# Kernel optimization log

Hardware: AMD Instinct MI355X
Metric: run time of the kernel (lower is better)

## Reference

```python
import jax, jax.numpy as jnp
import numpy as np

D_MODEL = 512
D_FF = 2048
N_EXPERTS = 8
TOP_K = 2
AUX_COEF = 0.01
Z_COEF = 1e-4
N_LAYERS = 12
INIT_STD = 0.02


def setup_inputs() -> dict:
    key = jax.random.key(0)
    kx, kr, k1, k2, k3 = jax.random.split(key, 5)
    std2 = INIT_STD / np.sqrt(2 * N_LAYERS)  # scale_init_by_depth for w2
    x = jax.random.normal(kx, (4, 1024, D_MODEL), dtype=jnp.float32)
    router_w = jax.random.normal(kr, (D_MODEL, N_EXPERTS), dtype=jnp.float32) * 0.02
    w1 = jax.random.normal(k1, (N_EXPERTS, D_MODEL, D_FF), dtype=jnp.float32) * INIT_STD
    w2 = jax.random.normal(k2, (N_EXPERTS, D_FF, D_MODEL), dtype=jnp.float32) * std2
    w3 = jax.random.normal(k3, (N_EXPERTS, D_MODEL, D_FF), dtype=jnp.float32) * INIT_STD
    return {"x": x, "router_w": router_w, "w1": w1, "w2": w2, "w3": w3}


def reference(x, router_w, w1, w2, w3):
    B, S, D = x.shape
    xf = x.reshape(-1, D)                              # [N, D]
    n_tokens = xf.shape[0]

    router_logits = xf @ router_w                      # [N, E]
    probs = jax.nn.softmax(router_logits.astype(jnp.float32), axis=-1)
    topk_w, topk_i = jax.lax.top_k(probs, TOP_K)       # [N, K]
    topk_w = topk_w / jnp.sum(topk_w, axis=-1, keepdims=True)

    # combine weight per (token, expert): zero for non-selected experts
    combine = jnp.sum(jax.nn.one_hot(topk_i, N_EXPERTS, dtype=jnp.float32)
                      * topk_w[..., None], axis=1)     # [N, E]

    # SwiGLU per expert, masked combine (same math as sorted grouped GEMM + scatter-add)
    gate = jax.nn.silu(jnp.einsum('nd,edf->enf', xf, w1))   # [E, N, F]
    up = jnp.einsum('nd,edf->enf', xf, w3)                  # [E, N, F]
    expert_out = jnp.einsum('enf,efd->end', gate * up, w2)  # [E, N, D]
    out = jnp.einsum('end,ne->nd', expert_out, combine.astype(x.dtype))

    # losses
    importance = probs.mean(axis=0)                    # [E]
    load = jax.nn.one_hot(topk_i[:, 0], N_EXPERTS, dtype=jnp.float32).mean(axis=0)
    aux_loss = N_EXPERTS * jnp.sum(importance * load) * AUX_COEF
    z_loss = jnp.mean(router_logits.astype(jnp.float32) ** 2) * Z_COEF

    return out.reshape(B, S, D), aux_loss, z_loss
```

## Files before the change

### kernel.cpp

```cpp
#include <hip/hip_runtime.h>
#include <hip/hip_fp16.h>

#define D_MODEL 512
#define D_FF    2048
#define NEXP    8
#define NTOK    4096
#define NPAIR   8192
#define DUMMY   NPAIR
#define LSTRIDE 4224
#define MAXTILES 72

typedef _Float16 half8  __attribute__((ext_vector_type(8)));
typedef _Float16 half2v __attribute__((ext_vector_type(2)));
typedef float    f32x4  __attribute__((ext_vector_type(4)));

__device__ __forceinline__ void gload16(const void* g, void* l) {
  __builtin_amdgcn_global_load_lds(
      (const __attribute__((address_space(1))) unsigned*)g,
      (__attribute__((address_space(3))) unsigned*)l, 16, 0, 0);
}

__global__ void k_trans3(const float* __restrict__ w1, const float* __restrict__ w3,
                         const float* __restrict__ w2, _Float16* __restrict__ w1t,
                         _Float16* __restrict__ w3t, _Float16* __restrict__ w2t) {
  __shared__ float t[64][65];
  int bt = blockIdx.x;
  const float* src; _Float16* dst; int R, C, rb, cb;
  if (bt < 4096) {
    src = (bt < 2048) ? w1 : w3; dst = (bt < 2048) ? w1t : w3t;
    int tt = bt & 2047; int e = tt >> 8; int rem = tt & 255;
    R = D_MODEL; C = D_FF; rb = (rem >> 5) * 64; cb = (rem & 31) * 64;
    src += (size_t)e * R * C; dst += (size_t)e * R * C;
  } else {
    int tt = bt - 4096; int e = tt >> 8; int rem = tt & 255;
    src = w2; dst = w2t;
    R = D_FF; C = D_MODEL; rb = (rem >> 3) * 64; cb = (rem & 7) * 64;
    src += (size_t)e * R * C; dst += (size_t)e * R * C;
  }
  int tid = threadIdx.x;
  int tx = tid & 15, ty = tid >> 4;
#pragma unroll
  for (int i = 0; i < 4; i++) {
    float4 v = *(const float4*)(src + (size_t)(rb + ty + i * 16) * C + cb + tx * 4);
    t[ty + i * 16][tx * 4 + 0] = v.x;
    t[ty + i * 16][tx * 4 + 1] = v.y;
    t[ty + i * 16][tx * 4 + 2] = v.z;
    t[ty + i * 16][tx * 4 + 3] = v.w;
  }
  __syncthreads();
  int tx2 = tid & 31, ty2 = tid >> 5;
#pragma unroll
  for (int i = 0; i < 8; i++) {
    int c = ty2 + i * 8;
    int r = tx2 * 2;
    half2v p = {(_Float16)t[r][c], (_Float16)t[r + 1][c]};
    *(half2v*)(dst + (size_t)(cb + c) * R + rb + r) = p;
  }
}

__global__ __launch_bounds__(256) void k_route1(
    const float* __restrict__ x, const float* __restrict__ rw,
    _Float16* __restrict__ xb, int* __restrict__ topE, float* __restrict__ wcomb,
    float* __restrict__ blk, int* __restrict__ ntiles) {
  __shared__ float s_imp[NEXP];
  __shared__ float s_z;
  int tid = threadIdx.x;
  if (tid < NEXP) s_imp[tid] = 0.f;
  if (tid == 0) s_z = 0.f;
  if (blockIdx.x == 0 && tid == 0) ntiles[0] = 0;
  __syncthreads();
  int wave = tid >> 6, lane = tid & 63;
  int n = blockIdx.x * 4 + wave;
  const float* xr = x + (size_t)n * D_MODEL;
  float acc[8] = {0, 0, 0, 0, 0, 0, 0, 0};
  float4 v0 = *(const float4*)(xr + lane * 8);
  float4 v1 = *(const float4*)(xr + lane * 8 + 4);
  float xs[8] = {v0.x, v0.y, v0.z, v0.w, v1.x, v1.y, v1.z, v1.w};
  half8 hx = {(_Float16)xs[0], (_Float16)xs[1], (_Float16)xs[2], (_Float16)xs[3],
              (_Float16)xs[4], (_Float16)xs[5], (_Float16)xs[6], (_Float16)xs[7]};
  *(half8*)(xb + (size_t)n * D_MODEL + lane * 8) = hx;
#pragma unroll
  for (int j = 0; j < 8; j++) {
    const float4* w4 = (const float4*)(rw + (size_t)(lane * 8 + j) * NEXP);
    float4 wa = w4[0], wb = w4[1];
    acc[0] += xs[j] * wa.x; acc[1] += xs[j] * wa.y;
    acc[2] += xs[j] * wa.z; acc[3] += xs[j] * wa.w;
    acc[4] += xs[j] * wb.x; acc[5] += xs[j] * wb.y;
    acc[6] += xs[j] * wb.z; acc[7] += xs[j] * wb.w;
  }
#pragma unroll
  for (int off = 32; off >= 1; off >>= 1) {
#pragma unroll
    for (int e = 0; e < 8; e++) acc[e] += __shfl_xor(acc[e], off);
  }
  if (lane == 0) {
    float z = 0.f;
#pragma unroll
    for (int e = 0; e < 8; e++) z += acc[e] * acc[e];
    float m = acc[0];
#pragma unroll
    for (int e = 1; e < 8; e++) m = fmaxf(m, acc[e]);
    float p[8], s = 0.f;
#pragma unroll
    for (int e = 0; e < 8; e++) { p[e] = expf(acc[e] - m); s += p[e]; }
    float inv = 1.f / s;
#pragma unroll
    for (int e = 0; e < 8; e++) p[e] *= inv;
    int e0 = 0; float p0 = p[0];
#pragma unroll
    for (int e = 1; e < 8; e++) if (p[e] > p0) { p0 = p[e]; e0 = e; }
    int e1 = -1; float p1 = -1.f;
#pragma unroll
    for (int e = 0; e < 8; e++) if (e != e0 && p[e] > p1) { p1 = p[e]; e1 = e; }
    float wsum = p0 + p1;
    topE[n] = e0 | (e1 << 4);
    wcomb[2 * n] = p0 / wsum;
    wcomb[2 * n + 1] = p1 / wsum;
#pragma unroll
    for (int e = 0; e < 8; e++) atomicAdd(&s_imp[e], p[e]);
    atomicAdd(&s_z, z);
  }
  __syncthreads();
  if (tid < 8) blk[blockIdx.x * 9 + tid] = s_imp[tid];
  if (tid == 8) blk[blockIdx.x * 9 + 8] = s_z;
}

__global__ __launch_bounds__(1024) void k_scatter(
    const int* __restrict__ topE, int* __restrict__ lists,
    int* __restrict__ tiletab, int* __restrict__ ntiles,
    int* __restrict__ loadc_g) {
  int e = blockIdx.x;
  __shared__ int wcount[16];
  __shared__ int lcw[16];
  __shared__ int sbase;
  __shared__ int stot;
  int tid = threadIdx.x, lane = tid & 63, wv = tid >> 6;
  if (lane == 0) lcw[wv] = 0;
  int total = 0;
  for (int c = 0; c < 8; c++) {
    int idx = c * 1024 + tid;
    int te = topE[idx >> 1];
    int ee = (idx & 1) ? ((te >> 4) & 15) : (te & 15);
    bool mine = (ee == e);
    unsigned long long bal = __ballot(mine);
    unsigned long long balL = __ballot(mine && !(idx & 1));
    int rank = __popcll(bal & ((1ull << lane) - 1ull));
    if (lane == 0) {
      wcount[wv] = __popcll(bal);
      lcw[wv] += __popcll(balL);
    }
    __syncthreads();
    int pre = total;
    for (int w2 = 0; w2 < wv; w2++) pre += wcount[w2];
    if (mine) lists[e * LSTRIDE + pre + rank] = idx;
    int t16 = 0;
#pragma unroll
    for (int w2 = 0; w2 < 16; w2++) t16 += wcount[w2];
    __syncthreads();
    total += t16;
  }
  int tiles = (total + 127) >> 7;
  if (tid == 0) {
    int lc = 0;
#pragma unroll
    for (int w2 = 0; w2 < 16; w2++) lc += lcw[w2];
    loadc_g[e] = lc;
    sbase = atomicAdd(ntiles, tiles);
    stot = total;
  }
  __syncthreads();
  if (tid < tiles) tiletab[sbase + tid] = e | (tid << 8);
  if (tid < 128) {
    int p = stot + tid;
    if (p < tiles * 128) lists[e * LSTRIDE + p] = DUMMY;
  }
}

__global__ __launch_bounds__(1024) void k_losses(
    const float* __restrict__ blk, const int* __restrict__ loadc_g,
    float* __restrict__ out) {
  __shared__ float fin[9];
  int tid = threadIdx.x, lane = tid & 63, wv = tid >> 6;
  if (wv < 9) {
    float s = 0.f;
    for (int b = lane; b < 1024; b += 64) s += blk[b * 9 + wv];
#pragma unroll
    for (int off = 32; off >= 1; off >>= 1) s += __shfl_xor(s, off);
    if (lane == 0) fin[wv] = s;
  }
  __syncthreads();
  if (tid == 0) {
    float a = 0.f;
#pragma unroll
    for (int e = 0; e < 8; e++)
      a += (fin[e] * (1.f / 4096.f)) * ((float)loadc_g[e] * (1.f / 4096.f));
    out[NTOK * D_MODEL] = 8.f * a * 0.01f;
    out[NTOK * D_MODEL + 1] = fin[8] * (1.f / (4096.f * 8.f)) * 1e-4f;
  }
}

__global__ __launch_bounds__(256) void k_gemm1(
    const _Float16* __restrict__ xb, const _Float16* __restrict__ w1t,
    const _Float16* __restrict__ w3t, _Float16* __restrict__ h,
    const int* __restrict__ lists, const int* __restrict__ tiletab,
    const int* __restrict__ ntiles) {
  int ti = blockIdx.y;
  if (ti >= ntiles[0]) return;
  int ent = tiletab[ti];
  int e = ent & 15, mt = ent >> 8, nt = blockIdx.x;
  __shared__ __align__(16) _Float16 As[2][128 * 32];
  __shared__ __align__(16) _Float16 B1s[2][128 * 32];
  __shared__ __align__(16) _Float16 B3s[2][128 * 32];
  __shared__ int toks[128];
  int tid = threadIdx.x, lane = tid & 63, w = tid >> 6;
  if (tid < 128) toks[tid] = lists[e * LSTRIDE + mt * 128 + tid];
  __syncthreads();
  const _Float16* w1e = w1t + (size_t)e * D_FF * D_MODEL;
  const _Float16* w3e = w3t + (size_t)e * D_FF * D_MODEL;
  int n0 = nt * 128;
  const _Float16 *aS[2], *b1S[2], *b3S[2];
  int ldso[2];
#pragma unroll
  for (int c = 0; c < 2; c++) {
    int rt = w * 32 + c * 16 + (lane >> 2);
    int cg = (lane & 3) ^ ((rt >> 1) & 3);
    aS[c] = xb + (size_t)(toks[rt] >> 1) * D_MODEL + cg * 8;
    b1S[c] = w1e + (size_t)(n0 + rt) * D_MODEL + cg * 8;
    b3S[c] = w3e + (size_t)(n0 + rt) * D_MODEL + cg * 8;
    ldso[c] = (w * 32 + c * 16) * 32;
  }
  f32x4 acc1[4][4] = {};
  f32x4 acc3[4][4] = {};
  int wr = (w >> 1) * 64, wc = (w & 1) * 64;
  int aoff[4], boff[4];
#pragma unroll
  for (int i = 0; i < 4; i++) {
    int r = wr + i * 16 + (lane & 15);
    aoff[i] = r * 32 + (((lane >> 4) ^ ((r >> 1) & 3)) << 3);
    int rb = wc + i * 16 + (lane & 15);
    boff[i] = rb * 32 + (((lane >> 4) ^ ((rb >> 1) & 3)) << 3);
  }
#pragma unroll
  for (int c = 0; c < 2; c++) {
    gload16(aS[c], &As[0][ldso[c]]);
    gload16(b1S[c], &B1s[0][ldso[c]]);
    gload16(b3S[c], &B3s[0][ldso[c]]);
  }
  __syncthreads();
#pragma unroll
  for (int t = 0; t < 16; t++) {
    const int buf = t & 1;
    if (t < 15) {
      const int k1 = (t + 1) * 32;
#pragma unroll
      for (int c = 0; c < 2; c++) {
        gload16(aS[c] + k1, &As[buf ^ 1][ldso[c]]);
        gload16(b1S[c] + k1, &B1s[buf ^ 1][ldso[c]]);
        gload16(b3S[c] + k1, &B3s[buf ^ 1][ldso[c]]);
      }
    }
    half8 af[4], b1f[4], b3f[4];
#pragma unroll
    for (int i = 0; i < 4; i++) {
      af[i] = *(const half8*)(&As[buf][aoff[i]]);
      b1f[i] = *(const half8*)(&B1s[buf][boff[i]]);
      b3f[i] = *(const half8*)(&B3s[buf][boff[i]]);
    }
#pragma unroll
    for (int i = 0; i < 4; i++) {
#pragma unroll
      for (int j = 0; j < 4; j++) {
        acc1[i][j] = __builtin_amdgcn_mfma_f32_16x16x32_f16(af[i], b1f[j], acc1[i][j], 0, 0, 0);
        acc3[i][j] = __builtin_amdgcn_mfma_f32_16x16x32_f16(af[i], b3f[j], acc3[i][j], 0, 0, 0);
      }
    }
    __syncthreads();
  }
#pragma unroll
  for (int i = 0; i < 4; i++) {
    int rbase = wr + i * 16 + ((lane >> 4) << 2);
#pragma unroll
    for (int r = 0; r < 4; r++) {
      int m = rbase + r;
      int pair = toks[m];
      _Float16* hrow = h + (size_t)pair * D_FF + n0 + wc;
#pragma unroll
      for (int j = 0; j < 4; j++) {
        float g = acc1[i][j][r], u = acc3[i][j][r];
        float val = (g / (1.f + __expf(-g))) * u;
        hrow[j * 16 + (lane & 15)] = (_Float16)val;
      }
    }
  }
}

__global__ __launch_bounds__(256) void k_gemm2(
    const _Float16* __restrict__ h, const _Float16* __restrict__ w2t,
    float* __restrict__ pairout, const int* __restrict__ lists,
    const int* __restrict__ tiletab, const int* __restrict__ ntiles,
    const float* __restrict__ wcomb) {
  int ti = blockIdx.y;
  if (ti >= ntiles[0]) return;
  int ent = tiletab[ti];
  int e = ent & 15, mt = ent >> 8, nt = blockIdx.x;
  __shared__ __align__(16) _Float16 As[2][128 * 32];
  __shared__ __align__(16) _Float16 Bs[2][64 * 32];
  __shared__ int toks[128];
  __shared__ float wcs[128];
  int tid = threadIdx.x, lane = tid & 63, w = tid >> 6;
  if (tid < 128) {
    int p = lists[e * LSTRIDE + mt * 128 + tid];
    toks[tid] = p;
    wcs[tid] = (p < NPAIR) ? wcomb[p] : 0.f;
  }
  __syncthreads();
  const _Float16* w2e = w2t + (size_t)e * D_MODEL * D_FF;
  int n0 = nt * 64;
  const _Float16 *aS[2], *bS;
  int ldsa[2], ldsb;
#pragma unroll
  for (int c = 0; c < 2; c++) {
    int rt = w * 32 + c * 16 + (lane >> 2);
    int cg = (lane & 3) ^ ((rt >> 1) & 3);
    aS[c] = h + (size_t)toks[rt] * D_FF + cg * 8;
    ldsa[c] = (w * 32 + c * 16) * 32;
  }
  {
    int rt = w * 16 + (lane >> 2);
    int cg = (lane & 3) ^ ((rt >> 1) & 3);
    bS = w2e + (size_t)(n0 + rt) * D_FF + cg * 8;
    ldsb = (w * 16) * 32;
  }
  f32x4 acc[4][2] = {};
  int wr = (w >> 1) * 64, wc = (w & 1) * 32;
  int aoff[4], boff[2];
#pragma unroll
  for (int i = 0; i < 4; i++) {
    int r = wr + i * 16 + (lane & 15);
    aoff[i] = r * 32 + (((lane >> 4) ^ ((r >> 1) & 3)) << 3);
  }
#pragma unroll
  for (int j = 0; j < 2; j++) {
    int r = wc + j * 16 + (lane & 15);
    boff[j] = r * 32 + (((lane >> 4) ^ ((r >> 1) & 3)) << 3);
  }
#pragma unroll
  for (int c = 0; c < 2; c++) gload16(aS[c], &As[0][ldsa[c]]);
  gload16(bS, &Bs[0][ldsb]);
  __syncthreads();
  for (int kk = 0; kk < D_FF; kk += 64) {
    {
#pragma unroll
      for (int c = 0; c < 2; c++) gload16(aS[c] + kk + 32, &As[1][ldsa[c]]);
      gload16(bS + kk + 32, &Bs[1][ldsb]);
      half8 af[4], bf[2];
#pragma unroll
      for (int i = 0; i < 4; i++) af[i] = *(const half8*)(&As[0][aoff[i]]);
#pragma unroll
      for (int j = 0; j < 2; j++) bf[j] = *(const half8*)(&Bs[0][boff[j]]);
#pragma unroll
      for (int i = 0; i < 4; i++)
#pragma unroll
        for (int j = 0; j < 2; j++)
          acc[i][j] = __builtin_amdgcn_mfma_f32_16x16x32_f16(af[i], bf[j], acc[i][j], 0, 0, 0);
      __syncthreads();
    }
    {
      if (kk + 64 < D_FF) {
#pragma unroll
        for (int c = 0; c < 2; c++) gload16(aS[c] + kk + 64, &As[0][ldsa[c]]);
        gload16(bS + kk + 64, &Bs[0][ldsb]);
      }
      half8 af[4], bf[2];
#pragma unroll
      for (int i = 0; i < 4; i++) af[i] = *(const half8*)(&As[1][aoff[i]]);
#pragma unroll
      for (int j = 0; j < 2; j++) bf[j] = *(const half8*)(&Bs[1][boff[j]]);
#pragma unroll
      for (int i = 0; i < 4; i++)
#pragma unroll
        for (int j = 0; j < 2; j++)
          acc[i][j] = __builtin_amdgcn_mfma_f32_16x16x32_f16(af[i], bf[j], acc[i][j], 0, 0, 0);
      __syncthreads();
    }
  }
#pragma unroll
  for (int i = 0; i < 4; i++) {
    int rbase = wr + i * 16 + ((lane >> 4) << 2);
#pragma unroll
    for (int r = 0; r < 4; r++) {
      int m = rbase + r;
      int pair = toks[m];
      float wv_ = wcs[m];
      float* orow = pairout + (size_t)pair * D_MODEL + n0 + wc;
#pragma unroll
      for (int j = 0; j < 2; j++)
        orow[j * 16 + (lane & 15)] = acc[i][j][r] * wv_;
    }
  }
}

__global__ void k_combine(const float* __restrict__ po, float* __restrict__ out) {
  int gid = blockIdx.x * blockDim.x + threadIdx.x;
  int r = gid >> 7;
  int c = (gid & 127) * 4;
  const float4 a = *(const float4*)(po + (size_t)(2 * r) * D_MODEL + c);
  const float4 b = *(const float4*)(po + (size_t)(2 * r + 1) * D_MODEL + c);
  float4 o{a.x + b.x, a.y + b.y, a.z + b.z, a.w + b.w};
  *(float4*)(out + (size_t)r * D_MODEL + c) = o;
}

extern "C" void kernel_launch(void* const* d_in, const int* in_sizes, int n_in,
                              void* d_out, int out_size, void* d_ws, size_t ws_size,
                              hipStream_t stream) {
  const float* x = (const float*)d_in[0];
  const float* rw = (const float*)d_in[1];
  const float* w1 = (const float*)d_in[2];
  const float* w2 = (const float*)d_in[3];
  const float* w3 = (const float*)d_in[4];
  float* out = (float*)d_out;

  char* ws = (char*)d_ws;
  size_t o = 0;
  _Float16* w1t = (_Float16*)(ws + o); o += (size_t)NEXP * D_FF * D_MODEL * 2;
  _Float16* w3t = (_Float16*)(ws + o); o += (size_t)NEXP * D_FF * D_MODEL * 2;
  _Float16* w2t = (_Float16*)(ws + o); o += (size_t)NEXP * D_MODEL * D_FF * 2;
  _Float16* xb = (_Float16*)(ws + o); o += (size_t)(NTOK + 1) * D_MODEL * 2;
  _Float16* hbuf = (_Float16*)(ws + o); o += (size_t)(NPAIR + 1) * D_FF * 2;
  int* lists = (int*)(ws + o); o += (size_t)NEXP * LSTRIDE * 4;
  float* wcomb = (float*)(ws + o); o += (size_t)NPAIR * 4;
  int* topE = (int*)(ws + o); o += (size_t)NTOK * 4;
  float* blk = (float*)(ws + o); o += (size_t)1024 * 9 * 4;
  int* tiletab = (int*)(ws + o); o += MAXTILES * 4;
  int* ntiles = (int*)(ws + o); o += 16;
  int* loadc_g = (int*)(ws + o); o += 64;
  float* pairout = (float*)ws;
  if (ws_size < o) return;

  k_route1<<<NTOK / 4, 256, 0, stream>>>(x, rw, xb, topE, wcomb, blk, ntiles);
  k_trans3<<<6144, 256, 0, stream>>>(w1, w3, w2, w1t, w3t, w2t);
  k_scatter<<<NEXP, 1024, 0, stream>>>(topE, lists, tiletab, ntiles, loadc_g);
  k_losses<<<1, 1024, 0, stream>>>(blk, loadc_g, out);
  k_gemm1<<<dim3(D_FF / 128, MAXTILES), 256, 0, stream>>>(xb, w1t, w3t, hbuf, lists, tiletab, ntiles);
  k_gemm2<<<dim3(D_MODEL / 64, MAXTILES), 256, 0, stream>>>(hbuf, w2t, pairout, lists, tiletab, ntiles, wcomb);
  k_combine<<<(NTOK * D_MODEL / 4 + 255) / 256, 256, 0, stream>>>(pairout, out);
}
```

Baseline: 299.9 us.

## Triple-buffer GEMM LDS pipelines with vmcnt waits and merge prep kernels

Both grouped GEMM kernels move from double to triple buffering in LDS. Each iteration uses a single barrier guarded by a partial s_waitcnt vmcnt, so two stages of global-to-LDS loads stay in flight while MFMAs run, instead of waiting on every load before a full __syncthreads. The routing kernel and the weight-transpose kernel are also merged into one launch to save a kernel launch. The cost is more LDS per block (gemm1 goes to about 72KB), which may reduce occupancy, and the vmcnt counts are hand-tuned to the number of loads issued per stage.

```diff
diff --git a/kernel.cpp b/kernel.cpp
--- a/kernel.cpp
+++ b/kernel.cpp
@@ -20,109 +20,117 @@
       (__attribute__((address_space(3))) unsigned*)l, 16, 0, 0);
 }
 
-__global__ void k_trans3(const float* __restrict__ w1, const float* __restrict__ w3,
-                         const float* __restrict__ w2, _Float16* __restrict__ w1t,
-                         _Float16* __restrict__ w3t, _Float16* __restrict__ w2t) {
+#define PIPE_BARRIER(N) do { \
+  asm volatile("s_waitcnt vmcnt(" #N ")" ::: "memory"); \
+  __builtin_amdgcn_s_barrier(); \
+  asm volatile("" ::: "memory"); \
+} while (0)
+
+__global__ __launch_bounds__(256) void k_prep(
+    const float* __restrict__ x, const float* __restrict__ rw,
+    const float* __restrict__ w1, const float* __restrict__ w3,
+    const float* __restrict__ w2, _Float16* __restrict__ w1t,
+    _Float16* __restrict__ w3t, _Float16* __restrict__ w2t,
+    _Float16* __restrict__ xb, int* __restrict__ topE,
+    float* __restrict__ wcomb, float* __restrict__ blk,
+    int* __restrict__ ntiles) {
   __shared__ float t[64][65];
-  int bt = blockIdx.x;
-  const float* src; _Float16* dst; int R, C, rb, cb;
-  if (bt < 4096) {
-    src = (bt < 2048) ? w1 : w3; dst = (bt < 2048) ? w1t : w3t;
-    int tt = bt & 2047; int e = tt >> 8; int rem = tt & 255;
-    R = D_MODEL; C = D_FF; rb = (rem >> 5) * 64; cb = (rem & 31) * 64;
-    src += (size_t)e * R * C; dst += (size_t)e * R * C;
+  int tid = threadIdx.x;
+  if (blockIdx.x < 6144) {
+    int bt = blockIdx.x;
+    const float* src; _Float16* dst; int R, C, rb, cb;
+    if (bt < 4096) {
+      src = (bt < 2048) ? w1 : w3; dst = (bt < 2048) ? w1t : w3t;
+      int tt = bt & 2047; int e = tt >> 8; int rem = tt & 255;
+      R = D_MODEL; C = D_FF; rb = (rem >> 5) * 64; cb = (rem & 31) * 64;
+      src += (size_t)e * R * C; dst += (size_t)e * R * C;
+    } else {
+      int tt = bt - 4096; int e = tt >> 8; int rem = tt & 255;
+      src = w2; dst = w2t;
+      R = D_FF; C = D_MODEL; rb = (rem >> 3) * 64; cb = (rem & 7) * 64;
+      src += (size_t)e * R * C; dst += (size_t)e * R * C;
+    }
+    int tx = tid & 15, ty = tid >> 4;
+#pragma unroll
+    for (int i = 0; i < 4; i++) {
+      float4 v = *(const float4*)(src + (size_t)(rb + ty + i * 16) * C + cb + tx * 4);
+      t[ty + i * 16][tx * 4 + 0] = v.x;
+      t[ty + i * 16][tx * 4 + 1] = v.y;
+      t[ty + i * 16][tx * 4 + 2] = v.z;
+      t[ty + i * 16][tx * 4 + 3] = v.w;
+    }
+    __syncthreads();
+    int tx2 = tid & 31, ty2 = tid >> 5;
+#pragma unroll
+    for (int i = 0; i < 8; i++) {
+      int c = ty2 + i * 8;
+      int r = tx2 * 2;
+      half2v p = {(_Float16)t[r][c], (_Float16)t[r + 1][c]};
+      *(half2v*)(dst + (size_t)(cb + c) * R + rb + r) = p;
+    }
   } else {
-    int tt = bt - 4096; int e = tt >> 8; int rem = tt & 255;
-    src = w2; dst = w2t;
-    R = D_FF; C = D_MODEL; rb = (rem >> 3) * 64; cb = (rem & 7) * 64;
-    src += (size_t)e * R * C; dst += (size_t)e * R * C;
-  }
-  int tid = threadIdx.x;
-  int tx = tid & 15, ty = tid >> 4;
-#pragma unroll
-  for (int i = 0; i < 4; i++) {
-    float4 v = *(const float4*)(src + (size_t)(rb + ty + i * 16) * C + cb + tx * 4);
-    t[ty + i * 16][tx * 4 + 0] = v.x;
-    t[ty + i * 16][tx * 4 + 1] = v.y;
-    t[ty + i * 16][tx * 4 + 2] = v.z;
-    t[ty + i * 16][tx * 4 + 3] = v.w;
-  }
-  __syncthreads();
-  int tx2 = tid & 31, ty2 = tid >> 5;
-#pragma unroll
-  for (int i = 0; i < 8; i++) {
-    int c = ty2 + i * 8;
-    int r = tx2 * 2;
-    half2v p = {(_Float16)t[r][c], (_Float16)t[r + 1][c]};
-    *(half2v*)(dst + (size_t)(cb + c) * R + rb + r) = p;
-  }
-}
-
-__global__ __launch_bounds__(256) void k_route1(
-    const float* __restrict__ x, const float* __restrict__ rw,
-    _Float16* __restrict__ xb, int* __restrict__ topE, float* __restrict__ wcomb,
-    float* __restrict__ blk, int* __restrict__ ntiles) {
-  __shared__ float s_imp[NEXP];
-  __shared__ float s_z;
-  int tid = threadIdx.x;
-  if (tid < NEXP) s_imp[tid] = 0.f;
-  if (tid == 0) s_z = 0.f;
-  if (blockIdx.x == 0 && tid == 0) ntiles[0] = 0;
-  __syncthreads();
-  int wave = tid >> 6, lane = tid & 63;
-  int n = blockIdx.x * 4 + wave;
-  const float* xr = x + (size_t)n * D_MODEL;
-  float acc[8] = {0, 0, 0, 0, 0, 0, 0, 0};
-  float4 v0 = *(const float4*)(xr + lane * 8);
-  float4 v1 = *(const float4*)(xr + lane * 8 + 4);
-  float xs[8] = {v0.x, v0.y, v0.z, v0.w, v1.x, v1.y, v1.z, v1.w};
-  half8 hx = {(_Float16)xs[0], (_Float16)xs[1], (_Float16)xs[2], (_Float16)xs[3],
-              (_Float16)xs[4], (_Float16)xs[5], (_Float16)xs[6], (_Float16)xs[7]};
-  *(half8*)(xb + (size_t)n * D_MODEL + lane * 8) = hx;
-#pragma unroll
-  for (int j = 0; j < 8; j++) {
-    const float4* w4 = (const float4*)(rw + (size_t)(lane * 8 + j) * NEXP);
-    float4 wa = w4[0], wb = w4[1];
-    acc[0] += xs[j] * wa.x; acc[1] += xs[j] * wa.y;
-    acc[2] += xs[j] * wa.z; acc[3] += xs[j] * wa.w;
-    acc[4] += xs[j] * wb.x; acc[5] += xs[j] * wb.y;
-    acc[6] += xs[j] * wb.z; acc[7] += xs[j] * wb.w;
-  }
-#pragma unroll
-  for (int off = 32; off >= 1; off >>= 1) {
-#pragma unroll
-    for (int e = 0; e < 8; e++) acc[e] += __shfl_xor(acc[e], off);
-  }
-  if (lane == 0) {
-    float z = 0.f;
-#pragma unroll
-    for (int e = 0; e < 8; e++) z += acc[e] * acc[e];
-    float m = acc[0];
-#pragma unroll
-    for (int e = 1; e < 8; e++) m = fmaxf(m, acc[e]);
-    float p[8], s = 0.f;
-#pragma unroll
-    for (int e = 0; e < 8; e++) { p[e] = expf(acc[e] - m); s += p[e]; }
-    float inv = 1.f / s;
-#pragma unroll
-    for (int e = 0; e < 8; e++) p[e] *= inv;
-    int e0 = 0; float p0 = p[0];
-#pragma unroll
-    for (int e = 1; e < 8; e++) if (p[e] > p0) { p0 = p[e]; e0 = e; }
-    int e1 = -1; float p1 = -1.f;
-#pragma unroll
-    for (int e = 0; e < 8; e++) if (e != e0 && p[e] > p1) { p1 = p[e]; e1 = e; }
-    float wsum = p0 + p1;
-    topE[n] = e0 | (e1 << 4);
-    wcomb[2 * n] = p0 / wsum;
-    wcomb[2 * n + 1] = p1 / wsum;
-#pragma unroll
-    for (int e = 0; e < 8; e++) atomicAdd(&s_imp[e], p[e]);
-    atomicAdd(&s_z, z);
-  }
-  __syncthreads();
-  if (tid < 8) blk[blockIdx.x * 9 + tid] = s_imp[tid];
-  if (tid == 8) blk[blockIdx.x * 9 + 8] = s_z;
+    int bx = blockIdx.x - 6144;
+    __shared__ float s_imp[NEXP];
+    __shared__ float s_z;
+    if (tid < NEXP) s_imp[tid] = 0.f;
+    if (tid == 0) s_z = 0.f;
+    if (bx == 0 && tid == 0) ntiles[0] = 0;
+    __syncthreads();
+    int wave = tid >> 6, lane = tid & 63;
+    int n = bx * 4 + wave;
+    const float* xr = x + (size_t)n * D_MODEL;
+    float acc[8] = {0, 0, 0, 0, 0, 0, 0, 0};
+    float4 v0 = *(const float4*)(xr + lane * 8);
+    float4 v1 = *(const float4*)(xr + lane * 8 + 4);
+    float xs[8] = {v0.x, v0.y, v0.z, v0.w, v1.x, v1.y, v1.z, v1.w};
+    half8 hx = {(_Float16)xs[0], (_Float16)xs[1], (_Float16)xs[2], (_Float16)xs[3],
+                (_Float16)xs[4], (_Float16)xs[5], (_Float16)xs[6], (_Float16)xs[7]};
+    *(half8*)(xb + (size_t)n * D_MODEL + lane * 8) = hx;
+#pragma unroll
+    for (int j = 0; j < 8; j++) {
+      const float4* w4 = (const float4*)(rw + (size_t)(lane * 8 + j) * NEXP);
+      float4 wa = w4[0], wb = w4[1];
+      acc[0] += xs[j] * wa.x; acc[1] += xs[j] * wa.y;
+      acc[2] += xs[j] * wa.z; acc[3] += xs[j] * wa.w;
+      acc[4] += xs[j] * wb.x; acc[5] += xs[j] * wb.y;
+      acc[6] += xs[j] * wb.z; acc[7] += xs[j] * wb.w;
+    }
+#pragma unroll
+    for (int off = 32; off >= 1; off >>= 1) {
+#pragma unroll
+      for (int e = 0; e < 8; e++) acc[e] += __shfl_xor(acc[e], off);
+    }
+    if (lane == 0) {
+      float z = 0.f;
+#pragma unroll
+      for (int e = 0; e < 8; e++) z += acc[e] * acc[e];
+      float m = acc[0];
+#pragma unroll
+      for (int e = 1; e < 8; e++) m = fmaxf(m, acc[e]);
+      float p[8], s = 0.f;
+#pragma unroll
+      for (int e = 0; e < 8; e++) { p[e] = expf(acc[e] - m); s += p[e]; }
+      float inv = 1.f / s;
+#pragma unroll
+      for (int e = 0; e < 8; e++) p[e] *= inv;
+      int e0 = 0; float p0 = p[0];
+#pragma unroll
+      for (int e = 1; e < 8; e++) if (p[e] > p0) { p0 = p[e]; e0 = e; }
+      int e1 = -1; float p1 = -1.f;
+#pragma unroll
+      for (int e = 0; e < 8; e++) if (e != e0 && p[e] > p1) { p1 = p[e]; e1 = e; }
+      float wsum = p0 + p1;
+      topE[n] = e0 | (e1 << 4);
+      wcomb[2 * n] = p0 / wsum;
+      wcomb[2 * n + 1] = p1 / wsum;
+#pragma unroll
+      for (int e = 0; e < 8; e++) atomicAdd(&s_imp[e], p[e]);
+      atomicAdd(&s_z, z);
+    }
+    __syncthreads();
+    if (tid < 8) blk[bx * 9 + tid] = s_imp[tid];
+    if (tid == 8) blk[bx * 9 + 8] = s_z;
+  }
 }
 
 __global__ __launch_bounds__(1024) void k_scatter(
@@ -208,9 +216,9 @@
   if (ti >= ntiles[0]) return;
   int ent = tiletab[ti];
   int e = ent & 15, mt = ent >> 8, nt = blockIdx.x;
-  __shared__ __align__(16) _Float16 As[2][128 * 32];
-  __shared__ __align__(16) _Float16 B1s[2][128 * 32];
-  __shared__ __align__(16) _Float16 B3s[2][128 * 32];
+  __shared__ __align__(16) _Float16 As[3][128 * 32];
+  __shared__ __align__(16) _Float16 B1s[3][128 * 32];
+  __shared__ __align__(16) _Float16 B3s[3][128 * 32];
   __shared__ int toks[128];
   int tid = threadIdx.x, lane = tid & 63, w = tid >> 6;
   if (tid < 128) toks[tid] = lists[e * LSTRIDE + mt * 128 + tid];
@@ -240,25 +248,24 @@
     int rb = wc + i * 16 + (lane & 15);
     boff[i] = rb * 32 + (((lane >> 4) ^ ((rb >> 1) & 3)) << 3);
   }
-#pragma unroll
-  for (int c = 0; c < 2; c++) {
-    gload16(aS[c], &As[0][ldso[c]]);
-    gload16(b1S[c], &B1s[0][ldso[c]]);
-    gload16(b3S[c], &B3s[0][ldso[c]]);
-  }
-  __syncthreads();
+#define G1_STAGE(T, BUF) do { \
+  _Pragma("unroll") \
+  for (int c = 0; c < 2; c++) { \
+    gload16(aS[c] + (T) * 32, &As[BUF][ldso[c]]); \
+    gload16(b1S[c] + (T) * 32, &B1s[BUF][ldso[c]]); \
+    gload16(b3S[c] + (T) * 32, &B3s[BUF][ldso[c]]); \
+  } } while (0)
+  G1_STAGE(0, 0);
+  G1_STAGE(1, 1);
 #pragma unroll
   for (int t = 0; t < 16; t++) {
-    const int buf = t & 1;
-    if (t < 15) {
-      const int k1 = (t + 1) * 32;
-#pragma unroll
-      for (int c = 0; c < 2; c++) {
-        gload16(aS[c] + k1, &As[buf ^ 1][ldso[c]]);
-        gload16(b1S[c] + k1, &B1s[buf ^ 1][ldso[c]]);
-        gload16(b3S[c] + k1, &B3s[buf ^ 1][ldso[c]]);
-      }
-    }
+    if (t < 15) PIPE_BARRIER(6);
+    else        PIPE_BARRIER(0);
+    if (t < 14) {
+      const int nb = (t + 2) % 3;
+      G1_STAGE(t + 2, nb);
+    }
+    const int buf = t % 3;
     half8 af[4], b1f[4], b3f[4];
 #pragma unroll
     for (int i = 0; i < 4; i++) {
@@ -274,8 +281,8 @@
         acc3[i][j] = __builtin_amdgcn_mfma_f32_16x16x32_f16(af[i], b3f[j], acc3[i][j], 0, 0, 0);
       }
     }
-    __syncthreads();
-  }
+  }
+#undef G1_STAGE
 #pragma unroll
   for (int i = 0; i < 4; i++) {
     int rbase = wr + i * 16 + ((lane >> 4) << 2);
@@ -303,8 +310,8 @@
   if (ti >= ntiles[0]) return;
   int ent = tiletab[ti];
   int e = ent & 15, mt = ent >> 8, nt = blockIdx.x;
-  __shared__ __align__(16) _Float16 As[2][128 * 32];
-  __shared__ __align__(16) _Float16 Bs[2][64 * 32];
+  __shared__ __align__(16) _Float16 As[3][128 * 32];
+  __shared__ __align__(16) _Float16 Bs[3][64 * 32];
   __shared__ int toks[128];
   __shared__ float wcs[128];
   int tid = threadIdx.x, lane = tid & 63, w = tid >> 6;
@@ -344,46 +351,34 @@
     int r = wc + j * 16 + (lane & 15);
     boff[j] = r * 32 + (((lane >> 4) ^ ((r >> 1) & 3)) << 3);
   }
-#pragma unroll
-  for (int c = 0; c < 2; c++) gload16(aS[c], &As[0][ldsa[c]]);
-  gload16(bS, &Bs[0][ldsb]);
-  __syncthreads();
-  for (int kk = 0; kk < D_FF; kk += 64) {
-    {
-#pragma unroll
-      for (int c = 0; c < 2; c++) gload16(aS[c] + kk + 32, &As[1][ldsa[c]]);
-      gload16(bS + kk + 32, &Bs[1][ldsb]);
-      half8 af[4], bf[2];
-#pragma unroll
-      for (int i = 0; i < 4; i++) af[i] = *(const half8*)(&As[0][aoff[i]]);
-#pragma unroll
-      for (int j = 0; j < 2; j++) bf[j] = *(const half8*)(&Bs[0][boff[j]]);
-#pragma unroll
-      for (int i = 0; i < 4; i++)
-#pragma unroll
-        for (int j = 0; j < 2; j++)
-          acc[i][j] = __builtin_amdgcn_mfma_f32_16x16x32_f16(af[i], bf[j], acc[i][j], 0, 0, 0);
-      __syncthreads();
-    }
-    {
-      if (kk + 64 < D_FF) {
-#pragma unroll
-        for (int c = 0; c < 2; c++) gload16(aS[c] + kk + 64, &As[0][ldsa[c]]);
-        gload16(bS + kk + 64, &Bs[0][ldsb]);
-      }
-      half8 af[4], bf[2];
-#pragma unroll
-      for (int i = 0; i < 4; i++) af[i] = *(const half8*)(&As[1][aoff[i]]);
-#pragma unroll
-      for (int j = 0; j < 2; j++) bf[j] = *(const half8*)(&Bs[1][boff[j]]);
-#pragma unroll
-      for (int i = 0; i < 4; i++)
-#pragma unroll
-        for (int j = 0; j < 2; j++)
-          acc[i][j] = __builtin_amdgcn_mfma_f32_16x16x32_f16(af[i], bf[j], acc[i][j], 0, 0, 0);
-      __syncthreads();
-    }
-  }
+#define G2_STAGE(T, BUF) do { \
+  _Pragma("unroll") \
+  for (int c = 0; c < 2; c++) gload16(aS[c] + (T) * 32, &As[BUF][ldsa[c]]); \
+  gload16(bS + (T) * 32, &Bs[BUF][ldsb]); \
+} while (0)
+  G2_STAGE(0, 0);
+  G2_STAGE(1, 1);
+#pragma unroll
+  for (int t = 0; t < 64; t++) {
+    if (t < 63) PIPE_BARRIER(3);
+    else        PIPE_BARRIER(0);
+    if (t < 62) {
+      const int nb = (t + 2) % 3;
+      G2_STAGE(t + 2, nb);
+    }
+    const int buf = t % 3;
+    half8 af[4], bf[2];
+#pragma unroll
+    for (int i = 0; i < 4; i++) af[i] = *(const half8*)(&As[buf][aoff[i]]);
+#pragma unroll
+    for (int j = 0; j < 2; j++) bf[j] = *(const half8*)(&Bs[buf][boff[j]]);
+#pragma unroll
+    for (int i = 0; i < 4; i++)
+#pragma unroll
+      for (int j = 0; j < 2; j++)
+        acc[i][j] = __builtin_amdgcn_mfma_f32_16x16x32_f16(af[i], bf[j], acc[i][j], 0, 0, 0);
+  }
+#undef G2_STAGE
 #pragma unroll
   for (int i = 0; i < 4; i++) {
     int rbase = wr + i * 16 + ((lane >> 4) << 2);
@@ -437,8 +432,8 @@
   float* pairout = (float*)ws;
   if (ws_size < o) return;
 
-  k_route1<<<NTOK / 4, 256, 0, stream>>>(x, rw, xb, topE, wcomb, blk, ntiles);
-  k_trans3<<<6144, 256, 0, stream>>>(w1, w3, w2, w1t, w3t, w2t);
+  k_prep<<<7168, 256, 0, stream>>>(x, rw, w1, w3, w2, w1t, w3t, w2t, xb, topE,
+                                   wcomb, blk, ntiles);
   k_scatter<<<NEXP, 1024, 0, stream>>>(topE, lists, tiletab, ntiles, loadc_g);
   k_losses<<<1, 1024, 0, stream>>>(blk, loadc_g, out);
   k_gemm1<<<dim3(D_FF / 128, MAXTILES), 256, 0, stream>>>(xb, w1t, w3t, hbuf, lists, tiletab, ntiles);
```

Result: no change. 294.1 us (-1.9%).
